# Kernel tuning notes

Measured on AMD Instinct MI355X. Metric: run time of the kernel, lower is better.

## Reference

```python
import jax, jax.numpy as jnp
import numpy as np
from jax import lax

WIRES = 4
EPS = 1e-5


def _conv2d(x, w, b):
    # x: [B,C,H,W], w: [O,I,3,3], SAME padding, stride 1
    y = lax.conv_general_dilated(x, w, (1, 1), 'SAME',
                                 dimension_numbers=('NCHW', 'OIHW', 'NCHW'))
    return y + b[None, :, None, None]


def _maxpool2(x):
    return lax.reduce_window(x, -jnp.inf, lax.max, (1, 1, 2, 2), (1, 1, 2, 2), 'VALID')


def _cnot_perm(c, t, n=WIRES):
    # wire 0 = most significant bit; CNOT is a self-inverse basis permutation
    idx = np.arange(2 ** n)
    cbit = (idx >> (n - 1 - c)) & 1
    flipped = idx ^ (1 << (n - 1 - t))
    return np.where(cbit == 1, flipped, idx)


_CNOT_PERMS = [_cnot_perm(c, c + 1) for c in range(WIRES - 1)]
_Z_SIGNS = np.stack([1.0 - 2.0 * ((np.arange(2 ** WIRES) >> (WIRES - 1 - i)) & 1)
                     for i in range(WIRES)], axis=1).astype(np.float32)  # [16, 4]


def _quantum_circuit(q_params, feats):
    # Batched state-vector sim of: RY(feats[i]) wire i; RX(params[i]) wire i;
    # CNOT chain; <Z_i>.  feats: [B,4], q_params: [4]
    hf = 0.5 * feats
    hp = 0.5 * q_params
    cy, sy = jnp.cos(hf), jnp.sin(hf)            # [B,4]
    cx, sx = jnp.cos(hp), jnp.sin(hp)            # [4]
    # per-wire state after RX @ RY |0>: amplitudes of |0>, |1>
    a0 = (cx * cy - 1j * sx * sy).astype(jnp.complex64)  # [B,4]
    a1 = (cx * sy - 1j * sx * cy).astype(jnp.complex64)  # [B,4]
    single = jnp.stack([a0, a1], axis=-1)        # [B,4,2]
    # product state -> full 16-dim state via successive outer products
    psi = single[:, 0]                           # [B,2]
    for i in range(1, WIRES):
        psi = (psi[:, :, None] * single[:, i][:, None, :]).reshape(psi.shape[0], -1)
    # CNOT chain = fixed basis permutations
    for perm in _CNOT_PERMS:
        psi = psi[:, perm]                       # [B,16]
    probs = psi.real ** 2 + psi.imag ** 2        # [B,16]
    return probs @ jnp.asarray(_Z_SIGNS)         # [B,4]


def setup_inputs() -> dict:
    key = jax.random.key(0)
    ks = jax.random.split(key, 8)
    B, C, H, W = 512, 1, 128, 128
    return {
        'x': jax.random.normal(ks[0], (B, C, H, W), jnp.float32),
        'conv1_w': jax.random.normal(ks[1], (8, C, 3, 3), jnp.float32) * 0.1,
        'conv1_b': jnp.zeros((8,), jnp.float32),
        'conv2_w': jax.random.normal(ks[2], (16, 8, 3, 3), jnp.float32) * 0.1,
        'conv2_b': jnp.zeros((16,), jnp.float32),
        'q_params': jax.random.normal(ks[3], (WIRES,), jnp.float32),
        'bn_gamma': jnp.ones((4,), jnp.float32),
        'bn_beta': jnp.zeros((4,), jnp.float32),
        'head_w': jax.random.normal(ks[4], (4, WIRES), jnp.float32) * 0.5,
        'head_b': jnp.zeros((4,), jnp.float32),
    }


def reference(x, conv1_w, conv1_b, conv2_w, conv2_b, q_params,
              bn_gamma, bn_beta, head_w, head_b):
    h = jax.nn.relu(_conv2d(x, conv1_w, conv1_b))
    h = _maxpool2(h)
    h = jax.nn.relu(_conv2d(h, conv2_w, conv2_b))
    h = _maxpool2(h)
    feats = h.mean(axis=(2, 3))                  # AdaptiveAvgPool2d(1) -> [B,16]
    q_out = _quantum_circuit(q_params, feats[:, :WIRES])  # [B,4]
    # BatchNorm1d (training mode, biased variance)
    mu = q_out.mean(axis=0)
    var = q_out.var(axis=0)
    normed = bn_gamma * (q_out - mu) / jnp.sqrt(var + EPS) + bn_beta
    return normed @ head_w.T + head_b
```

## Files before the change

kernel.cpp:

```cpp
#include <hip/hip_runtime.h>

#define EPS 1e-5f

typedef float f2 __attribute__((ext_vector_type(2)));
typedef float f4 __attribute__((ext_vector_type(4)));

__device__ __forceinline__ float uload(const float* __restrict__ p) {
  return __int_as_float(__builtin_amdgcn_readfirstlane(__float_as_int(*p)));
}

__device__ __forceinline__ f2 fma2(f2 a, f2 b, f2 c) {
  return __builtin_elementwise_fma(a, b, c);
}
__device__ __forceinline__ f2 splat2(float s) { f2 r; r.x = s; r.y = s; return r; }

__global__ __launch_bounds__(256, 4) void k12_fused(
    const float* __restrict__ x, const float* __restrict__ w1,
    const float* __restrict__ b1, const float* __restrict__ w2,
    const float* __restrict__ b2, float* __restrict__ partials) {
  __shared__ __align__(16) float p1[8][18][66];
  __shared__ __align__(16) float w1t[80];
  __shared__ __align__(16) float w2t[292];
  __shared__ float wred[4][4];

  const int q   = blockIdx.x & 3;
  const int b   = blockIdx.x >> 2;
  const int tid = threadIdx.x;
  const float* xb = x + (size_t)b * (128 * 128);

  auto c1_load = [&](int pos, float xin[4][6]) {
    const int gl = pos >> 5, i = pos & 31;
    const int G  = 16 * q - 1 + gl;
    const bool vG = ((unsigned)G) < 64u;
    const int xr0 = 2 * G - 1;
#pragma unroll
    for (int r = 0; r < 4; ++r) {
      const int row  = xr0 + r;
      const bool rok = vG && ((unsigned)row < 128u);
      const int rowc = min(max(row, 0), 127);
      const float* rp = xb + rowc * 128;
      const float le = rp[(i == 0) ? 0 : (4 * i - 1)];
      const f4 mid   = *(const f4*)(rp + 4 * i);
      const float ri = rp[(i == 31) ? 127 : (4 * i + 4)];
      xin[r][0] = (rok && i != 0)  ? le    : 0.f;
      xin[r][1] = rok              ? mid.x : 0.f;
      xin[r][2] = rok              ? mid.y : 0.f;
      xin[r][3] = rok              ? mid.z : 0.f;
      xin[r][4] = rok              ? mid.w : 0.f;
      xin[r][5] = (rok && i != 31) ? ri    : 0.f;
    }
  };
  auto c1_compute = [&](int pos, const float xin[4][6]) {
    const int gl = pos >> 5, i = pos & 31;
    const int G  = 16 * q - 1 + gl;
    const bool vG = ((unsigned)G) < 64u;
#pragma unroll 1
    for (int g = 0; g < 2; ++g) {
      f4 wq[9];
#pragma unroll
      for (int k = 0; k < 9; ++k) wq[k] = *(const f4*)&w1t[k * 8 + 4 * g];
      const f4 b4 = *(const f4*)&w1t[72 + 4 * g];
      const f2 bias0 = b4.xy, bias1 = b4.zw;
#pragma unroll
      for (int p = 0; p < 2; ++p)
#pragma unroll
        for (int h = 0; h < 2; ++h) {
          f2 best = splat2(0.f);
#pragma unroll
          for (int dy = 0; dy < 2; ++dy)
#pragma unroll
            for (int dx = 0; dx < 2; ++dx) {
              f2 a = p ? bias1 : bias0;
#pragma unroll
              for (int ky = 0; ky < 3; ++ky)
#pragma unroll
                for (int kx = 0; kx < 3; ++kx) {
                  const f2 wp = p ? wq[ky * 3 + kx].zw : wq[ky * 3 + kx].xy;
                  a = fma2(wp, splat2(xin[dy + ky][2 * h + dx + kx]), a);
                }
              best.x = fmaxf(best.x, a.x);
              best.y = fmaxf(best.y, a.y);
            }
          const int oc0 = 4 * g + 2 * p;
          p1[oc0][gl][2 * i + 1 + h]     = vG ? best.x : 0.f;
          p1[oc0 + 1][gl][2 * i + 1 + h] = vG ? best.y : 0.f;
        }
    }
  };

  if (tid < 72) {
    int oc = tid / 9, k = tid % 9;
    w1t[k * 8 + oc] = w1[tid];
  } else if (tid < 80) {
    w1t[tid] = b1[tid - 72];
  }
  {
    int t = tid;
    {
      int oc = t / 72, rem = t % 72, ic = rem / 9, k = rem % 9;
      w2t[(ic * 9 + k) * 4 + oc] = w2[t];
    }
    t = tid + 256;
    if (t < 288) {
      int oc = t / 72, rem = t % 72, ic = rem / 9, k = rem % 9;
      w2t[(ic * 9 + k) * 4 + oc] = w2[t];
    }
  }
  if (tid >= 80 && tid < 84) w2t[288 + tid - 80] = b2[tid - 80];
  if (tid >= 96 && tid < 240) {
    int t = tid - 96;
    int ic = t / 18, r = t % 18;
    p1[ic][r][0]  = 0.f;
    p1[ic][r][65] = 0.f;
  }

  float xin0[4][6];
  c1_load(tid, xin0);
  __syncthreads();

  c1_compute(tid, xin0);
#pragma unroll 1
  for (int pos = tid + 256; pos < 576; pos += 256) {
    float xin[4][6];
    c1_load(pos, xin);
    c1_compute(pos, xin);
  }
  __syncthreads();

  const int px2  = tid & 31;
  const int py2l = tid >> 5;

  f2 acc[2][2][2];
#pragma unroll
  for (int p = 0; p < 2; ++p) {
    const f2 bias = *(const f2*)&w2t[288 + 2 * p];
    acc[p][0][0] = bias; acc[p][0][1] = bias;
    acc[p][1][0] = bias; acc[p][1][1] = bias;
  }

  auto ld_xin = [&](int ic, float xin[4][4]) {
#pragma unroll
    for (int r = 0; r < 4; ++r) {
      const f2* rp = (const f2*)&p1[ic][2 * py2l + r][2 * px2];
      f2 v0 = rp[0], v1 = rp[1];
      xin[r][0] = v0.x; xin[r][1] = v0.y; xin[r][2] = v1.x; xin[r][3] = v1.y;
    }
  };
  auto c2_acc = [&](int ic, const float xin[4][4]) {
#pragma unroll
    for (int ky = 0; ky < 3; ++ky)
#pragma unroll
      for (int kx = 0; kx < 3; ++kx) {
        const int k = ky * 3 + kx;
        const f4 wv = *(const f4*)&w2t[(ic * 9 + k) * 4];
        const f2 wA = wv.xy, wB = wv.zw;
#pragma unroll
        for (int dy = 0; dy < 2; ++dy)
#pragma unroll
          for (int dx = 0; dx < 2; ++dx) {
            const f2 xs = splat2(xin[dy + ky][dx + kx]);
            acc[0][dy][dx] = fma2(wA, xs, acc[0][dy][dx]);
            acc[1][dy][dx] = fma2(wB, xs, acc[1][dy][dx]);
          }
      }
  };

  float xina[4][4], xinb[4][4];
  ld_xin(0, xina);
#pragma unroll 1
  for (int ic = 0; ic < 8; ic += 2) {
    ld_xin(ic + 1, xinb);
    c2_acc(ic, xina);
    if (ic < 6) ld_xin(ic + 2, xina);
    c2_acc(ic + 1, xinb);
  }

  const int lane = tid & 63, w = tid >> 6;
#pragma unroll
  for (int p = 0; p < 2; ++p) {
    f2 m01;
    m01.x = fmaxf(fmaxf(fmaxf(acc[p][0][0].x, acc[p][0][1].x),
                        fmaxf(acc[p][1][0].x, acc[p][1][1].x)), 0.f);
    m01.y = fmaxf(fmaxf(fmaxf(acc[p][0][0].y, acc[p][0][1].y),
                        fmaxf(acc[p][1][0].y, acc[p][1][1].y)), 0.f);
#pragma unroll
    for (int off = 32; off > 0; off >>= 1) {
      m01.x += __shfl_down(m01.x, off);
      m01.y += __shfl_down(m01.y, off);
    }
    if (lane == 0) { wred[w][2 * p] = m01.x; wred[w][2 * p + 1] = m01.y; }
  }
  __syncthreads();
  if (tid < 4) {
    float s = wred[0][tid] + wred[1][tid] + wred[2][tid] + wred[3][tid];
    partials[((size_t)b * 4 + q) * 4 + tid] = s;
  }
}

__global__ __launch_bounds__(512) void k3_tail(
    const float* __restrict__ partials, const float* __restrict__ qp,
    const float* __restrict__ gamma, const float* __restrict__ beta,
    const float* __restrict__ hw, const float* __restrict__ hb,
    float* __restrict__ out) {
  __shared__ float wsum[8][8];
  __shared__ float stats[8];
  const int tid = threadIdx.x;

  const f4* pp = (const f4*)(partials + tid * 16);
  f4 s0 = pp[0], s1 = pp[1], s2 = pp[2], s3 = pp[3];
  float f[4];
  f[0] = (s0.x + s1.x + s2.x + s3.x) * (1.f / 1024.f);
  f[1] = (s0.y + s1.y + s2.y + s3.y) * (1.f / 1024.f);
  f[2] = (s0.z + s1.z + s2.z + s3.z) * (1.f / 1024.f);
  f[3] = (s0.w + s1.w + s2.w + s3.w) * (1.f / 1024.f);

  float a0r[4], a0i[4], a1r[4], a1i[4];
#pragma unroll
  for (int i = 0; i < 4; ++i) {
    float cy, sy, cx, sx;
    __sincosf(0.5f * f[i], &sy, &cy);
    __sincosf(0.5f * uload(qp + i), &sx, &cx);
    a0r[i] = cx * cy; a0i[i] = -sx * sy;
    a1r[i] = cx * sy; a1i[i] = -sx * cy;
  }

  float pr[16], pi[16];
#pragma unroll
  for (int j = 0; j < 16; ++j) {
    float rr = 1.f, ii = 0.f;
#pragma unroll
    for (int w = 0; w < 4; ++w) {
      int bit = (j >> (3 - w)) & 1;
      float ar = bit ? a1r[w] : a0r[w];
      float ai = bit ? a1i[w] : a0i[w];
      float t = rr * ar - ii * ai;
      ii = rr * ai + ii * ar;
      rr = t;
    }
    pr[j] = rr; pi[j] = ii;
  }

  constexpr int comp[16] = {0, 1, 3, 2, 6, 7, 5, 4, 12, 13, 15, 14, 10, 11, 9, 8};
  float qv[4] = {0.f, 0.f, 0.f, 0.f};
#pragma unroll
  for (int j = 0; j < 16; ++j) {
    int s = comp[j];
    float p = pr[s] * pr[s] + pi[s] * pi[s];
#pragma unroll
    for (int i = 0; i < 4; ++i)
      qv[i] += ((j >> (3 - i)) & 1) ? -p : p;
  }

  float v[8];
#pragma unroll
  for (int i = 0; i < 4; ++i) { v[i] = qv[i]; v[4 + i] = qv[i] * qv[i]; }
#pragma unroll
  for (int k = 0; k < 8; ++k)
#pragma unroll
    for (int off = 32; off > 0; off >>= 1) v[k] += __shfl_down(v[k], off);
  const int lane = tid & 63, w = tid >> 6;
  if (lane == 0) {
#pragma unroll
    for (int k = 0; k < 8; ++k) wsum[w][k] = v[k];
  }
  __syncthreads();
  if (tid < 8) {
    float s = 0.f;
#pragma unroll
    for (int ww = 0; ww < 8; ++ww) s += wsum[ww][tid];
    stats[tid] = s * (1.f / 512.f);
  }
  __syncthreads();

  float nm[4];
#pragma unroll
  for (int i = 0; i < 4; ++i) {
    float mu  = stats[i];
    float var = stats[4 + i] - mu * mu;
    nm[i] = uload(gamma + i) * (qv[i] - mu) * rsqrtf(var + EPS) + uload(beta + i);
  }
#pragma unroll
  for (int k = 0; k < 4; ++k) {
    float o = uload(hb + k);
#pragma unroll
    for (int i = 0; i < 4; ++i) o = fmaf(nm[i], uload(hw + k * 4 + i), o);
    out[tid * 4 + k] = o;
  }
}

extern "C" void kernel_launch(void* const* d_in, const int* in_sizes, int n_in,
                              void* d_out, int out_size, void* d_ws, size_t ws_size,
                              hipStream_t stream) {
  const float* x  = (const float*)d_in[0];
  const float* w1 = (const float*)d_in[1];
  const float* b1 = (const float*)d_in[2];
  const float* w2 = (const float*)d_in[3];
  const float* b2 = (const float*)d_in[4];
  const float* qp = (const float*)d_in[5];
  const float* gm = (const float*)d_in[6];
  const float* bt = (const float*)d_in[7];
  const float* hw = (const float*)d_in[8];
  const float* hb = (const float*)d_in[9];
  float* out = (float*)d_out;

  float* partials = (float*)d_ws;

  k12_fused<<<512 * 4, 256, 0, stream>>>(x, w1, b1, w2, b2, partials);
  k3_tail<<<1, 512, 0, stream>>>(partials, qp, gm, bt, hw, hb, out);
}
```

Before: 122.0 us.

## Split each image into eight row strips and divide conv2 channels across thread groups

The fused conv kernel now launches eight blocks per image instead of four, so each block handles an 8-row pooled strip and its LDS tile shrinks. Within a block, conv2 work is divided by output-channel pair across two thread halves instead of every thread computing both pairs. The tail kernel is updated to sum eight partials per image. The aim is more blocks, lower LDS use and fewer registers per thread for better occupancy, at the cost of more halo recomputation of conv1 rows and a larger grid.

New measurement: 130.7 us. 1.07x slower.

```diff
diff --git a/kernel.cpp b/kernel.cpp
--- a/kernel.cpp
+++ b/kernel.cpp
@@ -18,19 +18,19 @@
     const float* __restrict__ x, const float* __restrict__ w1,
     const float* __restrict__ b1, const float* __restrict__ w2,
     const float* __restrict__ b2, float* __restrict__ partials) {
-  __shared__ __align__(16) float p1[8][18][66];
+  __shared__ __align__(16) float p1[8][10][66];
   __shared__ __align__(16) float w1t[80];
   __shared__ __align__(16) float w2t[292];
-  __shared__ float wred[4][4];
-
-  const int q   = blockIdx.x & 3;
-  const int b   = blockIdx.x >> 2;
+  __shared__ float wred[4][2];
+
+  const int q   = blockIdx.x & 7;
+  const int b   = blockIdx.x >> 3;
   const int tid = threadIdx.x;
   const float* xb = x + (size_t)b * (128 * 128);
 
   auto c1_load = [&](int pos, float xin[4][6]) {
     const int gl = pos >> 5, i = pos & 31;
-    const int G  = 16 * q - 1 + gl;
+    const int G  = 8 * q - 1 + gl;
     const bool vG = ((unsigned)G) < 64u;
     const int xr0 = 2 * G - 1;
 #pragma unroll
@@ -52,7 +52,7 @@
   };
   auto c1_compute = [&](int pos, const float xin[4][6]) {
     const int gl = pos >> 5, i = pos & 31;
-    const int G  = 16 * q - 1 + gl;
+    const int G  = 8 * q - 1 + gl;
     const bool vG = ((unsigned)G) < 64u;
 #pragma unroll 1
     for (int g = 0; g < 2; ++g) {
@@ -107,9 +107,9 @@
     }
   }
   if (tid >= 80 && tid < 84) w2t[288 + tid - 80] = b2[tid - 80];
-  if (tid >= 96 && tid < 240) {
+  if (tid >= 96 && tid < 176) {
     int t = tid - 96;
-    int ic = t / 18, r = t % 18;
+    int ic = t / 10, r = t % 10;
     p1[ic][r][0]  = 0.f;
     p1[ic][r][65] = 0.f;
   }
@@ -119,23 +119,22 @@
   __syncthreads();
 
   c1_compute(tid, xin0);
-#pragma unroll 1
-  for (int pos = tid + 256; pos < 576; pos += 256) {
+  if (tid < 64) {
     float xin[4][6];
-    c1_load(pos, xin);
-    c1_compute(pos, xin);
+    c1_load(tid + 256, xin);
+    c1_compute(tid + 256, xin);
   }
   __syncthreads();
 
   const int px2  = tid & 31;
-  const int py2l = tid >> 5;
-
-  f2 acc[2][2][2];
-#pragma unroll
-  for (int p = 0; p < 2; ++p) {
-    const f2 bias = *(const f2*)&w2t[288 + 2 * p];
-    acc[p][0][0] = bias; acc[p][0][1] = bias;
-    acc[p][1][0] = bias; acc[p][1][1] = bias;
+  const int py2l = (tid >> 5) & 3;
+  const int g2   = tid >> 7;
+
+  f2 acc[2][2];
+  {
+    const f2 bias = *(const f2*)&w2t[288 + 2 * g2];
+    acc[0][0] = bias; acc[0][1] = bias;
+    acc[1][0] = bias; acc[1][1] = bias;
   }
 
   auto ld_xin = [&](int ic, float xin[4][4]) {
@@ -153,14 +152,12 @@
       for (int kx = 0; kx < 3; ++kx) {
         const int k = ky * 3 + kx;
         const f4 wv = *(const f4*)&w2t[(ic * 9 + k) * 4];
-        const f2 wA = wv.xy, wB = wv.zw;
+        const f2 wp = g2 ? wv.zw : wv.xy;
 #pragma unroll
         for (int dy = 0; dy < 2; ++dy)
 #pragma unroll
           for (int dx = 0; dx < 2; ++dx) {
-            const f2 xs = splat2(xin[dy + ky][dx + kx]);
-            acc[0][dy][dx] = fma2(wA, xs, acc[0][dy][dx]);
-            acc[1][dy][dx] = fma2(wB, xs, acc[1][dy][dx]);
+            acc[dy][dx] = fma2(wp, splat2(xin[dy + ky][dx + kx]), acc[dy][dx]);
           }
       }
   };
@@ -176,24 +173,24 @@
   }
 
   const int lane = tid & 63, w = tid >> 6;
-#pragma unroll
-  for (int p = 0; p < 2; ++p) {
+  {
     f2 m01;
-    m01.x = fmaxf(fmaxf(fmaxf(acc[p][0][0].x, acc[p][0][1].x),
-                        fmaxf(acc[p][1][0].x, acc[p][1][1].x)), 0.f);
-    m01.y = fmaxf(fmaxf(fmaxf(acc[p][0][0].y, acc[p][0][1].y),
-                        fmaxf(acc[p][1][0].y, acc[p][1][1].y)), 0.f);
+    m01.x = fmaxf(fmaxf(fmaxf(acc[0][0].x, acc[0][1].x),
+                        fmaxf(acc[1][0].x, acc[1][1].x)), 0.f);
+    m01.y = fmaxf(fmaxf(fmaxf(acc[0][0].y, acc[0][1].y),
+                        fmaxf(acc[1][0].y, acc[1][1].y)), 0.f);
 #pragma unroll
     for (int off = 32; off > 0; off >>= 1) {
       m01.x += __shfl_down(m01.x, off);
       m01.y += __shfl_down(m01.y, off);
     }
-    if (lane == 0) { wred[w][2 * p] = m01.x; wred[w][2 * p + 1] = m01.y; }
+    if (lane == 0) { wred[w][0] = m01.x; wred[w][1] = m01.y; }
   }
   __syncthreads();
   if (tid < 4) {
-    float s = wred[0][tid] + wred[1][tid] + wred[2][tid] + wred[3][tid];
-    partials[((size_t)b * 4 + q) * 4 + tid] = s;
+    const int wbase = (tid >> 1) * 2, c = tid & 1;
+    float s = wred[wbase][c] + wred[wbase + 1][c];
+    partials[((size_t)b * 8 + q) * 4 + tid] = s;
   }
 }
 
@@ -206,13 +203,15 @@
   __shared__ float stats[8];
   const int tid = threadIdx.x;
 
-  const f4* pp = (const f4*)(partials + tid * 16);
-  f4 s0 = pp[0], s1 = pp[1], s2 = pp[2], s3 = pp[3];
-  float f[4];
-  f[0] = (s0.x + s1.x + s2.x + s3.x) * (1.f / 1024.f);
-  f[1] = (s0.y + s1.y + s2.y + s3.y) * (1.f / 1024.f);
-  f[2] = (s0.z + s1.z + s2.z + s3.z) * (1.f / 1024.f);
-  f[3] = (s0.w + s1.w + s2.w + s3.w) * (1.f / 1024.f);
+  const f4* pp = (const f4*)(partials + tid * 32);
+  float f[4] = {0.f, 0.f, 0.f, 0.f};
+#pragma unroll
+  for (int s = 0; s < 8; ++s) {
+    f4 v = pp[s];
+    f[0] += v.x; f[1] += v.y; f[2] += v.z; f[3] += v.w;
+  }
+#pragma unroll
+  for (int i = 0; i < 4; ++i) f[i] *= (1.f / 1024.f);
 
   float a0r[4], a0i[4], a1r[4], a1i[4];
 #pragma unroll
@@ -305,6 +304,6 @@
 
   float* partials = (float*)d_ws;
 
-  k12_fused<<<512 * 4, 256, 0, stream>>>(x, w1, b1, w2, b2, partials);
+  k12_fused<<<512 * 8, 256, 0, stream>>>(x, w1, b1, w2, b2, partials);
   k3_tail<<<1, 512, 0, stream>>>(partials, qp, gm, bt, hw, hb, out);
 }
```
